# Kernel tuning notes

Hardware: AMD Instinct MI355X
Metric: run time of the kernel (lower is better)

The kernel has to match this reference:

```python
import jax, jax.numpy as jnp
import numpy as np

K_EXPERTS = 2  # init kwarg k_experts

def _glu_mlp(x, up_w, gate_w, down_w):
    # gated MLP: down( up(x) * GELU(gate(x)) ), exact-erf GELU matching torch nn.GELU()
    h = (x @ up_w) * jax.nn.gelu(x @ gate_w, approximate=False)
    return h @ down_w

def setup_inputs() -> dict:
    key = jax.random.key(0)
    ks = jax.random.split(key, 8)
    B, S, D, I, E = 2, 2048, 1024, 512, 8
    sc = 0.02
    return {
        "x": jax.random.normal(ks[0], (B, S, D), jnp.float32),
        "gate_w": jax.random.normal(ks[1], (E, D), jnp.float32) * sc,
        "up_w": jax.random.normal(ks[2], (E, D, I), jnp.float32) * sc,
        "gproj_w": jax.random.normal(ks[3], (E, D, I), jnp.float32) * sc,
        "down_w": jax.random.normal(ks[4], (E, I, D), jnp.float32) * sc,
        "shared_up_w": jax.random.normal(ks[5], (D, I), jnp.float32) * sc,
        "shared_gate_w": jax.random.normal(ks[6], (D, I), jnp.float32) * sc,
        "shared_down_w": jax.random.normal(ks[7], (I, D), jnp.float32) * sc,
    }

def reference(x, gate_w, up_w, gproj_w, down_w, shared_up_w, shared_gate_w, shared_down_w):
    B, S, D = x.shape
    E = gate_w.shape[0]
    xf = x.reshape(-1, D)                      # [T, D]
    T = xf.shape[0]

    # --- SigmaGate: softmax over expert logits, top-k, renormalize ---
    logits = xf @ gate_w.T                     # [T, E]
    scores = jax.nn.softmax(logits, axis=-1)
    topk_w, topk_idx = jax.lax.top_k(scores, K_EXPERTS)   # [T, k]
    topk_w = topk_w / (topk_w.sum(axis=-1, keepdims=True) + 1e-20)

    # combine weights as dense [T, E] (topk indices are distinct per token)
    combine = jnp.zeros((T, E), xf.dtype).at[jnp.arange(T)[:, None], topk_idx].add(topk_w)

    # --- experts: scan over E, accumulate weighted expert outputs ---
    def step(acc, ws):
        uw, gw, dw, ce = ws                    # ce: [T] combine weight for this expert
        y_e = _glu_mlp(xf, uw, gw, dw)         # [T, D]
        return acc + ce[:, None] * y_e, None

    y, _ = jax.lax.scan(step, jnp.zeros_like(xf), (up_w, gproj_w, down_w, combine.T))

    # --- shared expert on identity ---
    y = y + _glu_mlp(xf, shared_up_w, shared_gate_w, shared_down_w)
    return y.reshape(B, S, D)
```

## Files before the change

kernel.cpp:

```cpp
#include <hip/hip_runtime.h>
#include <hip/hip_bf16.h>
#include <math.h>

#define T_TOK 4096
#define D_DIM 1024
#define I_DIM 512
#define E_EXP 8
#define KSEL 2
#define NPAIR (T_TOK * KSEL)
#define ROUTED_CAP 9216
#define SHARED_BASE ROUTED_CAP
#define RTOT (ROUTED_CAP + T_TOK)
#define MAXTILES 104
#define GRID_G (MAXTILES * 8)

typedef __bf16 bf16x8 __attribute__((ext_vector_type(8)));
typedef float f32x4 __attribute__((ext_vector_type(4)));
typedef unsigned short ushort8 __attribute__((ext_vector_type(8)));

constexpr size_t SZ_XB  = (size_t)T_TOK * D_DIM * 2;
constexpr size_t SZ_UG  = (size_t)E_EXP * 2 * I_DIM * D_DIM * 2;
constexpr size_t SZ_DT  = (size_t)E_EXP * I_DIM * D_DIM * 2;
constexpr size_t SZ_SUG = (size_t)2 * I_DIM * D_DIM * 2;
constexpr size_t SZ_SDT = (size_t)I_DIM * D_DIM * 2;
constexpr size_t SZ_H   = (size_t)RTOT * I_DIM * 2;
constexpr size_t SZ_Y   = (size_t)RTOT * D_DIM * 2;

constexpr size_t OFF_XB   = 0;
constexpr size_t OFF_UG   = OFF_XB  + SZ_XB;
constexpr size_t OFF_DT   = OFF_UG  + SZ_UG;
constexpr size_t OFF_SUG  = OFF_DT  + SZ_DT;
constexpr size_t OFF_SDT  = OFF_SUG + SZ_SUG;
constexpr size_t OFF_H    = OFF_SDT + SZ_SDT;
constexpr size_t OFF_Y    = OFF_H   + SZ_H;
constexpr size_t OFF_TOPKI= OFF_Y   + SZ_Y;
constexpr size_t OFF_TOPKW= OFF_TOPKI + (size_t)NPAIR * 4;
constexpr size_t OFF_INV  = OFF_TOPKW + (size_t)NPAIR * 4;
constexpr size_t OFF_PERM = OFF_INV   + (size_t)NPAIR * 4;
constexpr size_t OFF_META = OFF_PERM  + (size_t)RTOT * 4;

__device__ __forceinline__ unsigned short f2bf(float f) {
  unsigned int u = __float_as_uint(f);
  unsigned int r = (u + 0x7FFFu + ((u >> 16) & 1u)) >> 16;
  return (unsigned short)r;
}
__device__ __forceinline__ float bf2f(unsigned short s) {
  return __uint_as_float(((unsigned int)s) << 16);
}
__device__ __forceinline__ void gload_lds16(const void* g, void* l) {
  __builtin_amdgcn_global_load_lds(
      (const __attribute__((address_space(1))) void*)g,
      (__attribute__((address_space(3))) void*)l, 16, 0, 0);
}

__global__ void transpose_cvt_all(
    const float* __restrict__ upw, const float* __restrict__ gpw,
    const float* __restrict__ dww, const float* __restrict__ sup,
    const float* __restrict__ sgt, const float* __restrict__ sdw,
    unsigned short* __restrict__ UG, unsigned short* __restrict__ sUG,
    unsigned short* __restrict__ Dt, unsigned short* __restrict__ sDt) {
  __shared__ float t[32][33];
  int bid = blockIdx.x;
  const float* in; unsigned short* out;
  int R, C, xt, yt, mode;
  if (bid < 4096)       { int e = bid >> 9, s = bid & 511;
    in = upw + (size_t)e * D_DIM * I_DIM; out = UG + (size_t)e * 2 * I_DIM * D_DIM;
    R = D_DIM; C = I_DIM; xt = s & 15; yt = s >> 4; mode = 0; }
  else if (bid < 8192)  { int b = bid - 4096; int e = b >> 9, s = b & 511;
    in = gpw + (size_t)e * D_DIM * I_DIM; out = UG + (size_t)e * 2 * I_DIM * D_DIM;
    R = D_DIM; C = I_DIM; xt = s & 15; yt = s >> 4; mode = 1; }
  else if (bid < 12288) { int b = bid - 8192; int e = b >> 9, s = b & 511;
    in = dww + (size_t)e * I_DIM * D_DIM; out = Dt + (size_t)e * I_DIM * D_DIM;
    R = I_DIM; C = D_DIM; xt = s & 31; yt = s >> 5; mode = 2; }
  else if (bid < 12800) { int s = bid - 12288;
    in = sup; out = sUG; R = D_DIM; C = I_DIM; xt = s & 15; yt = s >> 4; mode = 0; }
  else if (bid < 13312) { int s = bid - 12800;
    in = sgt; out = sUG; R = D_DIM; C = I_DIM; xt = s & 15; yt = s >> 4; mode = 1; }
  else                  { int s = bid - 13312;
    in = sdw; out = sDt; R = I_DIM; C = D_DIM; xt = s & 31; yt = s >> 5; mode = 2; }
  int c0 = xt * 32, r0 = yt * 32;
  int tx = threadIdx.x, ty = threadIdx.y;
#pragma unroll
  for (int i = 0; i < 4; ++i)
    t[ty + 8 * i][tx] = in[(size_t)(r0 + ty + 8 * i) * C + c0 + tx];
  __syncthreads();
#pragma unroll
  for (int i = 0; i < 4; ++i) {
    int c = c0 + ty + 8 * i;
    int orow = (mode == 2) ? c : (((c >> 4) << 5) + (c & 15) + (mode == 1 ? 16 : 0));
    out[(size_t)orow * R + r0 + tx] = f2bf(t[tx][ty + 8 * i]);
  }
}

__global__ void gating_kernel(const float* __restrict__ x, const float* __restrict__ gw,
                              unsigned short* __restrict__ xb,
                              int* __restrict__ topk_idx, float* __restrict__ topk_w) {
  int lane = threadIdx.x & 63;
  int t = blockIdx.x * 4 + (threadIdx.x >> 6);
  const float4* xr = (const float4*)(x + (size_t)t * D_DIM);
  float4 xv[4];
#pragma unroll
  for (int j = 0; j < 4; ++j) xv[j] = xr[lane + 64 * j];
#pragma unroll
  for (int j = 0; j < 4; ++j) {
    ushort4 o;
    o.x = f2bf(xv[j].x); o.y = f2bf(xv[j].y); o.z = f2bf(xv[j].z); o.w = f2bf(xv[j].w);
    *(ushort4*)&xb[(size_t)t * D_DIM + (lane + 64 * j) * 4] = o;
  }
  float acc[E_EXP];
#pragma unroll
  for (int e = 0; e < E_EXP; ++e) {
    const float4* gr = (const float4*)(gw + (size_t)e * D_DIM);
    float a = 0.f;
#pragma unroll
    for (int j = 0; j < 4; ++j) {
      float4 g = gr[lane + 64 * j];
      a += xv[j].x * g.x + xv[j].y * g.y + xv[j].z * g.z + xv[j].w * g.w;
    }
    acc[e] = a;
  }
#pragma unroll
  for (int off = 32; off; off >>= 1)
#pragma unroll
    for (int e = 0; e < E_EXP; ++e) acc[e] += __shfl_xor(acc[e], off, 64);
  if (lane == 0) {
    int i0 = 0; float m0 = acc[0];
#pragma unroll
    for (int e = 1; e < E_EXP; ++e) if (acc[e] > m0) { m0 = acc[e]; i0 = e; }
    int i1 = -1; float m1 = -1e30f;
#pragma unroll
    for (int e = 0; e < E_EXP; ++e) if (e != i0 && acc[e] > m1) { m1 = acc[e]; i1 = e; }
    float e1 = __expf(m1 - m0);
    float w0 = 1.0f / (1.0f + e1);
    float w1 = e1 / (1.0f + e1);
    topk_idx[2 * t] = i0; topk_idx[2 * t + 1] = i1;
    topk_w[2 * t] = w0;   topk_w[2 * t + 1] = w1;
  }
}

__global__ __launch_bounds__(1024) void route_kernel(
    const int* __restrict__ tidx, int* __restrict__ meta,
    int* __restrict__ perm, int* __restrict__ inv) {
  __shared__ int els[NPAIR];
  __shared__ int cnt_iw[128][E_EXP];
  __shared__ int base_iw[128][E_EXP];
  __shared__ int ebase[E_EXP];
  __shared__ int ecnt[E_EXP];
  int tid = threadIdx.x, lane = tid & 63, wv = tid >> 6;

  for (int it = 0; it < NPAIR / 1024; ++it) {
    int g = it * 1024 + tid;
    int e = tidx[g];
    els[g] = e;
#pragma unroll
    for (int ex = 0; ex < E_EXP; ++ex) {
      unsigned long long m = __ballot(e == ex);
      if (lane == 0) cnt_iw[it * 16 + wv][ex] = __popcll(m);
    }
  }
  __syncthreads();

  if (tid < E_EXP) {
    int s = 0;
    for (int iw = 0; iw < 128; ++iw) { base_iw[iw][tid] = s; s += cnt_iw[iw][tid]; }
    ecnt[tid] = s;
  }
  __syncthreads();

  if (tid == 0) {
    int o = 0, tc = 0;
    int2* m2 = (int2*)meta;
    for (int e = 0; e < E_EXP; ++e) {
      ebase[e] = o;
      int c = ecnt[e];
      int pt = (c + 127) >> 7;
      for (int ti = 0; ti < pt; ++ti) m2[tc++] = make_int2(e, o + ti * 128);
      o += pt * 128;
    }
    for (int ti = 0; ti < T_TOK / 128; ++ti)
      m2[tc++] = make_int2(E_EXP, SHARED_BASE + ti * 128);
    for (; tc < MAXTILES; ++tc) m2[tc] = make_int2(-1, 0);
  }
  __syncthreads();

  for (int it = 0; it < NPAIR / 1024; ++it) {
    int g = it * 1024 + tid;
    int e = els[g];
    int rank = 0;
#pragma unroll
    for (int ex = 0; ex < E_EXP; ++ex) {
      unsigned long long m = __ballot(e == ex);
      if (e == ex) rank = __popcll(m & ((1ull << lane) - 1ull));
    }
    int row = ebase[e] + base_iw[it * 16 + wv][e] + rank;
    perm[row] = g >> 1;
    inv[g] = row;
  }
  {
    int p = tid;
    int e = p >> 7, s = p & 127;
    int c = ecnt[e];
    int padn = (((c + 127) >> 7) << 7) - c;
    if (s < padn) perm[ebase[e] + c + s] = 0;
  }
  for (int t = tid; t < T_TOK; t += 1024) perm[SHARED_BASE + t] = t;
}

__global__ __launch_bounds__(256, 3) void gemm1_kernel(
    const unsigned short* __restrict__ xb, const unsigned short* __restrict__ UG,
    const unsigned short* __restrict__ sUG, unsigned short* __restrict__ H,
    const int* __restrict__ meta, const int* __restrict__ perm) {
  int orig = blockIdx.x;
  int wg = (orig & 7) * (GRID_G / 8) + (orig >> 3);
  int mt = wg >> 3, nt = wg & 7;
  int2 m2 = ((const int2*)meta)[mt];
  int e = m2.x;
  if (e < 0) return;
  int base = m2.y;
  int n0 = nt * 128;
  const unsigned short* B = (e < E_EXP) ? UG + (size_t)e * 2 * I_DIM * D_DIM : sUG;

  __shared__ unsigned short As[128 * 64];
  __shared__ unsigned short Bs[128 * 64];

  int tid = threadIdx.x, lane = tid & 63, wv = tid >> 6;
  const unsigned short *gA[4], *gB[4];
  unsigned short *lA[4], *lB[4];
#pragma unroll
  for (int j = 0; j < 4; ++j) {
    int c = j * 256 + tid;
    int row = c >> 3, q = c & 7, qs = q ^ (row & 7);
    int tok = perm[base + row];
    gA[j] = xb + (size_t)tok * D_DIM + qs * 8;
    gB[j] = B + (size_t)(n0 + row) * D_DIM + qs * 8;
    int dbase = (j * 256 + wv * 64) * 8;
    lA[j] = As + dbase; lB[j] = Bs + dbase;
  }

  f32x4 acc[4][4] = {};
  int wr = (wv >> 1) * 64, wc = (wv & 1) * 64;
  int l15 = lane & 15, l4 = lane >> 4;
  int sx = l15 & 7;

  for (int k0 = 0; k0 < D_DIM; k0 += 64) {
#pragma unroll
    for (int j = 0; j < 4; ++j) { gload_lds16(gA[j] + k0, lA[j]); gload_lds16(gB[j] + k0, lB[j]); }
    __syncthreads();
#pragma unroll
    for (int kh = 0; kh < 2; ++kh) {
      bf16x8 af[4], bf[4];
      int kb = kh * 4 + l4;
#pragma unroll
      for (int i = 0; i < 4; ++i) {
        af[i] = *reinterpret_cast<const bf16x8*>(&As[(wr + i * 16 + l15) * 64 + (kb ^ sx) * 8]);
        bf[i] = *reinterpret_cast<const bf16x8*>(&Bs[(wc + i * 16 + l15) * 64 + (kb ^ sx) * 8]);
      }
#pragma unroll
      for (int i = 0; i < 4; ++i)
#pragma unroll
        for (int j = 0; j < 4; ++j)
          acc[i][j] = __builtin_amdgcn_mfma_f32_16x16x32_bf16(af[i], bf[j], acc[i][j], 0, 0, 0);
    }
    __syncthreads();
  }

  const float is2 = 0.70710678118654752f;
  int hbase = (n0 >> 1) + (wv & 1) * 32;
#pragma unroll
  for (int i = 0; i < 4; ++i) {
    int row = base + wr + i * 16 + l4 * 4;
#pragma unroll
    for (int m = 0; m < 2; ++m) {
      int col = hbase + m * 16 + l15;
#pragma unroll
      for (int r = 0; r < 4; ++r) {
        float u = acc[i][2 * m][r], g = acc[i][2 * m + 1][r];
        float gl = 0.5f * g * (1.0f + erff(g * is2));
        H[(size_t)(row + r) * I_DIM + col] = f2bf(u * gl);
      }
    }
  }
}

__global__ __launch_bounds__(256, 3) void gemm2_kernel(
    const unsigned short* __restrict__ H, const unsigned short* __restrict__ Dt,
    const unsigned short* __restrict__ sDt, unsigned short* __restrict__ Y,
    const int* __restrict__ meta) {
  int orig = blockIdx.x;
  int wg = (orig & 7) * (GRID_G / 8) + (orig >> 3);
  int mt = wg >> 3, nt = wg & 7;
  int2 m2 = ((const int2*)meta)[mt];
  int e = m2.x;
  if (e < 0) return;
  int base = m2.y;
  int n0 = nt * 128;
  const unsigned short* B = (e < E_EXP) ? Dt + (size_t)e * D_DIM * I_DIM : sDt;

  __shared__ unsigned short As[128 * 64];
  __shared__ unsigned short Bs[128 * 64];

  int tid = threadIdx.x, lane = tid & 63, wv = tid >> 6;
  const unsigned short *gA[4], *gB[4];
  unsigned short *lA[4], *lB[4];
#pragma unroll
  for (int j = 0; j < 4; ++j) {
    int c = j * 256 + tid;
    int row = c >> 3, q = c & 7, qs = q ^ (row & 7);
    gA[j] = H + (size_t)(base + row) * I_DIM + qs * 8;
    gB[j] = B + (size_t)(n0 + row) * I_DIM + qs * 8;
    int dbase = (j * 256 + wv * 64) * 8;
    lA[j] = As + dbase; lB[j] = Bs + dbase;
  }

  f32x4 acc[4][4] = {};
  int wr = (wv >> 1) * 64, wc = (wv & 1) * 64;
  int l15 = lane & 15, l4 = lane >> 4;
  int sx = l15 & 7;

  for (int k0 = 0; k0 < I_DIM; k0 += 64) {
#pragma unroll
    for (int j = 0; j < 4; ++j) { gload_lds16(gA[j] + k0, lA[j]); gload_lds16(gB[j] + k0, lB[j]); }
    __syncthreads();
#pragma unroll
    for (int kh = 0; kh < 2; ++kh) {
      bf16x8 af[4], bf[4];
      int kb = kh * 4 + l4;
#pragma unroll
      for (int i = 0; i < 4; ++i) {
        af[i] = *reinterpret_cast<const bf16x8*>(&As[(wr + i * 16 + l15) * 64 + (kb ^ sx) * 8]);
        bf[i] = *reinterpret_cast<const bf16x8*>(&Bs[(wc + i * 16 + l15) * 64 + (kb ^ sx) * 8]);
      }
#pragma unroll
      for (int i = 0; i < 4; ++i)
#pragma unroll
        for (int j = 0; j < 4; ++j)
          acc[i][j] = __builtin_amdgcn_mfma_f32_16x16x32_bf16(af[i], bf[j], acc[i][j], 0, 0, 0);
    }
    __syncthreads();
  }

#pragma unroll
  for (int i = 0; i < 4; ++i) {
    int row = base + wr + i * 16 + l4 * 4;
#pragma unroll
    for (int j = 0; j < 4; ++j) {
      int col = n0 + wc + j * 16 + l15;
#pragma unroll
      for (int r = 0; r < 4; ++r)
        Y[(size_t)(row + r) * D_DIM + col] = f2bf(acc[i][j][r]);
    }
  }
}

__global__ void combine_kernel(const unsigned short* __restrict__ Y, const int* __restrict__ inv,
                               const float* __restrict__ tw, float* __restrict__ out) {
  int g = blockIdx.x * 256 + threadIdx.x;
  int t = g >> 7, d0 = (g & 127) * 8;
  int r0 = inv[2 * t], r1 = inv[2 * t + 1];
  float w0 = tw[2 * t], w1 = tw[2 * t + 1];
  ushort8 y0 = *(const ushort8*)&Y[(size_t)r0 * D_DIM + d0];
  ushort8 y1 = *(const ushort8*)&Y[(size_t)r1 * D_DIM + d0];
  ushort8 ys = *(const ushort8*)&Y[(size_t)(SHARED_BASE + t) * D_DIM + d0];
  float o[8];
#pragma unroll
  for (int j = 0; j < 8; ++j)
    o[j] = w0 * bf2f(y0[j]) + w1 * bf2f(y1[j]) + bf2f(ys[j]);
  float4* op = (float4*)(out + (size_t)t * D_DIM + d0);
  op[0] = make_float4(o[0], o[1], o[2], o[3]);
  op[1] = make_float4(o[4], o[5], o[6], o[7]);
}

extern "C" void kernel_launch(void* const* d_in, const int* in_sizes, int n_in,
                              void* d_out, int out_size, void* d_ws, size_t ws_size,
                              hipStream_t stream) {
  const float* x    = (const float*)d_in[0];
  const float* gw   = (const float*)d_in[1];
  const float* upw  = (const float*)d_in[2];
  const float* gpw  = (const float*)d_in[3];
  const float* dww  = (const float*)d_in[4];
  const float* sup  = (const float*)d_in[5];
  const float* sgt  = (const float*)d_in[6];
  const float* sdw  = (const float*)d_in[7];
  float* out = (float*)d_out;

  char* ws = (char*)d_ws;
  unsigned short* xb  = (unsigned short*)(ws + OFF_XB);
  unsigned short* UG  = (unsigned short*)(ws + OFF_UG);
  unsigned short* Dt  = (unsigned short*)(ws + OFF_DT);
  unsigned short* sUG = (unsigned short*)(ws + OFF_SUG);
  unsigned short* sDt = (unsigned short*)(ws + OFF_SDT);
  unsigned short* H   = (unsigned short*)(ws + OFF_H);
  unsigned short* Y   = (unsigned short*)(ws + OFF_Y);
  int*   tki   = (int*)(ws + OFF_TOPKI);
  float* tkw   = (float*)(ws + OFF_TOPKW);
  int*   inv   = (int*)(ws + OFF_INV);
  int*   perm  = (int*)(ws + OFF_PERM);
  int*   meta  = (int*)(ws + OFF_META);

  transpose_cvt_all<<<13824, dim3(32, 8), 0, stream>>>(upw, gpw, dww, sup, sgt, sdw,
                                                       UG, sUG, Dt, sDt);
  gating_kernel<<<T_TOK / 4, 256, 0, stream>>>(x, gw, xb, tki, tkw);
  route_kernel<<<1, 1024, 0, stream>>>(tki, meta, perm, inv);

  gemm1_kernel<<<GRID_G, 256, 0, stream>>>(xb, UG, sUG, H, meta, perm);
  gemm2_kernel<<<GRID_G, 256, 0, stream>>>(H, Dt, sDt, Y, meta);
  combine_kernel<<<(T_TOK * 128) / 256, 256, 0, stream>>>(Y, inv, tkw, out);
}
```

Baseline: 113.0 us.

## Double-buffer LDS tiles in both expert GEMMs to overlap loads with MFMA

Both grouped GEMM kernels now use two LDS buffers per operand. The next K-tile's global-to-LDS loads are issued before computing on the current tile, with explicit vmcnt waits and raw barriers in place of __syncthreads. Fragments are read into registers before a barrier, and the MFMA block runs at raised wave priority. The aim is to hide global load latency behind matrix math; in exchange the doubled LDS footprint and extra fragment registers lower the occupancy target from 3 to 2 blocks per CU.

```diff
diff --git a/kernel.cpp b/kernel.cpp
--- a/kernel.cpp
+++ b/kernel.cpp
@@ -206,7 +206,7 @@
   for (int t = tid; t < T_TOK; t += 1024) perm[SHARED_BASE + t] = t;
 }
 
-__global__ __launch_bounds__(256, 3) void gemm1_kernel(
+__global__ __launch_bounds__(256, 2) void gemm1_kernel(
     const unsigned short* __restrict__ xb, const unsigned short* __restrict__ UG,
     const unsigned short* __restrict__ sUG, unsigned short* __restrict__ H,
     const int* __restrict__ meta, const int* __restrict__ perm) {
@@ -220,12 +220,12 @@
   int n0 = nt * 128;
   const unsigned short* B = (e < E_EXP) ? UG + (size_t)e * 2 * I_DIM * D_DIM : sUG;
 
-  __shared__ unsigned short As[128 * 64];
-  __shared__ unsigned short Bs[128 * 64];
+  __shared__ unsigned short As[2 * 128 * 64];
+  __shared__ unsigned short Bs[2 * 128 * 64];
 
   int tid = threadIdx.x, lane = tid & 63, wv = tid >> 6;
   const unsigned short *gA[4], *gB[4];
-  unsigned short *lA[4], *lB[4];
+  int dL[4];
 #pragma unroll
   for (int j = 0; j < 4; ++j) {
     int c = j * 256 + tid;
@@ -233,8 +233,7 @@
     int tok = perm[base + row];
     gA[j] = xb + (size_t)tok * D_DIM + qs * 8;
     gB[j] = B + (size_t)(n0 + row) * D_DIM + qs * 8;
-    int dbase = (j * 256 + wv * 64) * 8;
-    lA[j] = As + dbase; lB[j] = Bs + dbase;
+    dL[j] = (j * 256 + wv * 64) * 8;
   }
 
   f32x4 acc[4][4] = {};
@@ -242,27 +241,47 @@
   int l15 = lane & 15, l4 = lane >> 4;
   int sx = l15 & 7;
 
-  for (int k0 = 0; k0 < D_DIM; k0 += 64) {
-#pragma unroll
-    for (int j = 0; j < 4; ++j) { gload_lds16(gA[j] + k0, lA[j]); gload_lds16(gB[j] + k0, lB[j]); }
-    __syncthreads();
+#define STAGE1(buf, k0) do { \
+  _Pragma("unroll") \
+  for (int j = 0; j < 4; ++j) { \
+    gload_lds16(gA[j] + (k0), As + (buf) * 8192 + dL[j]); \
+    gload_lds16(gB[j] + (k0), Bs + (buf) * 8192 + dL[j]); \
+  } } while (0)
+
+  STAGE1(0, 0);
+  const int NK = D_DIM / 64;
+  for (int t = 0; t < NK; ++t) {
+    int cur = t & 1;
+    if (t + 1 < NK) {
+      STAGE1(cur ^ 1, (t + 1) * 64);
+      asm volatile("s_waitcnt vmcnt(8)" ::: "memory");
+    } else {
+      asm volatile("s_waitcnt vmcnt(0)" ::: "memory");
+    }
+    __builtin_amdgcn_s_barrier();
+    bf16x8 af[2][4], bfr[2][4];
 #pragma unroll
     for (int kh = 0; kh < 2; ++kh) {
-      bf16x8 af[4], bf[4];
       int kb = kh * 4 + l4;
 #pragma unroll
       for (int i = 0; i < 4; ++i) {
-        af[i] = *reinterpret_cast<const bf16x8*>(&As[(wr + i * 16 + l15) * 64 + (kb ^ sx) * 8]);
-        bf[i] = *reinterpret_cast<const bf16x8*>(&Bs[(wc + i * 16 + l15) * 64 + (kb ^ sx) * 8]);
+        af[kh][i]  = *reinterpret_cast<const bf16x8*>(&As[cur * 8192 + (wr + i * 16 + l15) * 64 + (kb ^ sx) * 8]);
+        bfr[kh][i] = *reinterpret_cast<const bf16x8*>(&Bs[cur * 8192 + (wc + i * 16 + l15) * 64 + (kb ^ sx) * 8]);
       }
+    }
+    asm volatile("" ::: "memory");
+    __builtin_amdgcn_s_barrier();
+    __builtin_amdgcn_s_setprio(1);
+#pragma unroll
+    for (int kh = 0; kh < 2; ++kh)
 #pragma unroll
       for (int i = 0; i < 4; ++i)
 #pragma unroll
         for (int j = 0; j < 4; ++j)
-          acc[i][j] = __builtin_amdgcn_mfma_f32_16x16x32_bf16(af[i], bf[j], acc[i][j], 0, 0, 0);
-    }
-    __syncthreads();
-  }
+          acc[i][j] = __builtin_amdgcn_mfma_f32_16x16x32_bf16(af[kh][i], bfr[kh][j], acc[i][j], 0, 0, 0);
+    __builtin_amdgcn_s_setprio(0);
+  }
+#undef STAGE1
 
   const float is2 = 0.70710678118654752f;
   int hbase = (n0 >> 1) + (wv & 1) * 32;
@@ -282,7 +301,7 @@
   }
 }
 
-__global__ __launch_bounds__(256, 3) void gemm2_kernel(
+__global__ __launch_bounds__(256, 2) void gemm2_kernel(
     const unsigned short* __restrict__ H, const unsigned short* __restrict__ Dt,
     const unsigned short* __restrict__ sDt, unsigned short* __restrict__ Y,
     const int* __restrict__ meta) {
@@ -296,20 +315,19 @@
   int n0 = nt * 128;
   const unsigned short* B = (e < E_EXP) ? Dt + (size_t)e * D_DIM * I_DIM : sDt;
 
-  __shared__ unsigned short As[128 * 64];
-  __shared__ unsigned short Bs[128 * 64];
+  __shared__ unsigned short As[2 * 128 * 64];
+  __shared__ unsigned short Bs[2 * 128 * 64];
 
   int tid = threadIdx.x, lane = tid & 63, wv = tid >> 6;
   const unsigned short *gA[4], *gB[4];
-  unsigned short *lA[4], *lB[4];
+  int dL[4];
 #pragma unroll
   for (int j = 0; j < 4; ++j) {
     int c = j * 256 + tid;
     int row = c >> 3, q = c & 7, qs = q ^ (row & 7);
     gA[j] = H + (size_t)(base + row) * I_DIM + qs * 8;
     gB[j] = B + (size_t)(n0 + row) * I_DIM + qs * 8;
-    int dbase = (j * 256 + wv * 64) * 8;
-    lA[j] = As + dbase; lB[j] = Bs + dbase;
+    dL[j] = (j * 256 + wv * 64) * 8;
   }
 
   f32x4 acc[4][4] = {};
@@ -317,27 +335,47 @@
   int l15 = lane & 15, l4 = lane >> 4;
   int sx = l15 & 7;
 
-  for (int k0 = 0; k0 < I_DIM; k0 += 64) {
-#pragma unroll
-    for (int j = 0; j < 4; ++j) { gload_lds16(gA[j] + k0, lA[j]); gload_lds16(gB[j] + k0, lB[j]); }
-    __syncthreads();
+#define STAGE2(buf, k0) do { \
+  _Pragma("unroll") \
+  for (int j = 0; j < 4; ++j) { \
+    gload_lds16(gA[j] + (k0), As + (buf) * 8192 + dL[j]); \
+    gload_lds16(gB[j] + (k0), Bs + (buf) * 8192 + dL[j]); \
+  } } while (0)
+
+  STAGE2(0, 0);
+  const int NK = I_DIM / 64;
+  for (int t = 0; t < NK; ++t) {
+    int cur = t & 1;
+    if (t + 1 < NK) {
+      STAGE2(cur ^ 1, (t + 1) * 64);
+      asm volatile("s_waitcnt vmcnt(8)" ::: "memory");
+    } else {
+      asm volatile("s_waitcnt vmcnt(0)" ::: "memory");
+    }
+    __builtin_amdgcn_s_barrier();
+    bf16x8 af[2][4], bfr[2][4];
 #pragma unroll
     for (int kh = 0; kh < 2; ++kh) {
-      bf16x8 af[4], bf[4];
       int kb = kh * 4 + l4;
 #pragma unroll
       for (int i = 0; i < 4; ++i) {
-        af[i] = *reinterpret_cast<const bf16x8*>(&As[(wr + i * 16 + l15) * 64 + (kb ^ sx) * 8]);
-        bf[i] = *reinterpret_cast<const bf16x8*>(&Bs[(wc + i * 16 + l15) * 64 + (kb ^ sx) * 8]);
+        af[kh][i]  = *reinterpret_cast<const bf16x8*>(&As[cur * 8192 + (wr + i * 16 + l15) * 64 + (kb ^ sx) * 8]);
+        bfr[kh][i] = *reinterpret_cast<const bf16x8*>(&Bs[cur * 8192 + (wc + i * 16 + l15) * 64 + (kb ^ sx) * 8]);
       }
+    }
+    asm volatile("" ::: "memory");
+    __builtin_amdgcn_s_barrier();
+    __builtin_amdgcn_s_setprio(1);
+#pragma unroll
+    for (int kh = 0; kh < 2; ++kh)
 #pragma unroll
       for (int i = 0; i < 4; ++i)
 #pragma unroll
         for (int j = 0; j < 4; ++j)
-          acc[i][j] = __builtin_amdgcn_mfma_f32_16x16x32_bf16(af[i], bf[j], acc[i][j], 0, 0, 0);
-    }
-    __syncthreads();
-  }
+          acc[i][j] = __builtin_amdgcn_mfma_f32_16x16x32_bf16(af[kh][i], bfr[kh][j], acc[i][j], 0, 0, 0);
+    __builtin_amdgcn_s_setprio(0);
+  }
+#undef STAGE2
 
 #pragma unroll
   for (int i = 0; i < 4; ++i) {
```

Result: faster. 110.5 us (-2.2%).
